# Performance work log

Measured on AMD Instinct MI355X. Metric: run time of the kernel, lower is better.

## Reference

```python
import jax, jax.numpy as jnp
import numpy as np

B, T, N, F = 8, 24, 207, 16
H = 64            # hidden_dim
DH = 16           # dims_hyper[-1] / node-embedding out
DA = 4 * F        # temporal attention dim_out
DS = 64           # ss_gal gcn out dim (last_ss_gal_dim)
GDEP = 2
ALPHA, BETA, GAMMA = 0.05, 0.95, 0.95
TA = 2.0


def _lin(x, w, b=None):
    y = x @ w
    return y if b is None else y + b


def gcn_hyper(x, A, W, b):
    # x: [B,N,C], A: [N,N] static. h <- a*x + g * einsum('nvc,vw->nwc', h, A)
    h = x
    outs = [h]
    for _ in range(GDEP):
        h = ALPHA * x + GAMMA * jnp.einsum('bvc,vw->bwc', h, A)
        outs.append(h)
    return _lin(jnp.concatenate(outs, axis=-1), W, b)


def gcn_gru(x, A_dyn, A_sta, W, b):
    # x: [B,N,C], A_dyn: [B,N,N], A_sta: [N,N]
    h = x
    outs = [h]
    for _ in range(GDEP):
        h = (ALPHA * x
             + BETA * jnp.einsum('bvw,bvc->bwc', A_dyn, h)     # bmm(A^T, h)
             + GAMMA * jnp.einsum('bvc,vw->bwc', h, A_sta))
        outs.append(h)
    return _lin(jnp.concatenate(outs, axis=-1), W, b)


def gcn_ssgal(x, A, W, b):
    # x: [B*,N,C], A: [B*,N,N]
    h = x
    outs = [h]
    for _ in range(GDEP):
        h = ALPHA * x + GAMMA * jnp.einsum('bvw,bvc->bwc', A, h)
        outs.append(h)
    return _lin(jnp.concatenate(outs, axis=-1), W, b)


def setup_inputs() -> dict:
    key = jax.random.key(0)
    ks = jax.random.split(key, 32)
    i = iter(range(32))
    w = lambda *s: (0.02 * jax.random.normal(ks[next(i)], s, dtype=jnp.float32))
    inp = {
        'input_sequence': jax.random.normal(ks[next(i)], (B, T, N, F), dtype=jnp.float32),
        'static_adj': jax.random.uniform(ks[next(i)], (N, N), dtype=jnp.float32),
        # hyper graph generators: mlp in = (GDEP+1)*H -> DH
        'src_gen_w': w((GDEP + 1) * H, DH), 'src_gen_b': w(DH),
        'tgt_gen_w': w((GDEP + 1) * H, DH), 'tgt_gen_b': w(DH),
        # node embeddings: F -> DH
        'src_emb_w': w(F, DH), 'src_emb_b': w(DH),
        'tgt_emb_w': w(F, DH), 'tgt_emb_b': w(DH),
        # GRU gate GCNs: mlp in = (GDEP+1)*(F+H) -> H
        'gru_z_w': w((GDEP + 1) * (F + H), H), 'gru_z_b': w(H),
        'gru_r_w': w((GDEP + 1) * (F + H), H), 'gru_r_b': w(H),
        'gru_c_w': w((GDEP + 1) * (F + H), H), 'gru_c_b': w(H),
        # temporal attention: F -> DA, score DA -> 1
        'attn_q_w': w(F, DA),
        'attn_k_w': w(F, DA), 'attn_k_b': w(DA),
        'attn_s_w': w(DA, 1),
        # ss_gal spatial gcn: (GDEP+1)*F -> DS
        'sgcn_w': w((GDEP + 1) * F, DS), 'sgcn_b': w(DS),
        # predictors
        'short_w': w(DS, F), 'short_b': w(F),
        'long_w': w(H, F), 'long_b': w(F),
        'fus_w': w(DS + H, F), 'fus_b': w(F),
    }
    return inp


def _forward(input_sequence, static_adj,
             src_gen_w, src_gen_b, tgt_gen_w, tgt_gen_b,
             src_emb_w, src_emb_b, tgt_emb_w, tgt_emb_b,
             gru_z_w, gru_z_b, gru_r_w, gru_r_b, gru_c_w, gru_c_b,
             attn_q_w, attn_k_w, attn_k_b, attn_s_w,
             sgcn_w, sgcn_b,
             short_w, short_b, long_w, long_b, fus_w, fus_b):
    batch, steps, nodes = input_sequence.shape[0], input_sequence.shape[1], input_sequence.shape[2]
    eye = jnp.eye(nodes, dtype=input_sequence.dtype)

    def cell(x_t, h):
        # x_t: [B,N,F], h: [B,N,H]
        src_ctx = gcn_hyper(h, static_adj, src_gen_w, src_gen_b)   # [B,N,DH]
        tgt_ctx = gcn_hyper(h, static_adj, tgt_gen_w, tgt_gen_b)
        s = jnp.tanh(TA * _lin(x_t, src_emb_w, src_emb_b) * src_ctx)
        t = jnp.tanh(TA * _lin(x_t, tgt_emb_w, tgt_emb_b) * tgt_ctx)
        asym = jnp.einsum('bnc,bmc->bnm', s, t) - jnp.einsum('bnc,bmc->bnm', t, s)
        adj = jax.nn.relu(jnp.tanh(TA * asym)) + eye
        adj = adj / (adj.sum(axis=-1, keepdims=True) + 1e-8)
        gi = jnp.concatenate([x_t, h], axis=-1)
        z = jax.nn.sigmoid(gcn_gru(gi, adj, static_adj, gru_z_w, gru_z_b))
        r = jax.nn.sigmoid(gcn_gru(gi, adj, static_adj, gru_r_w, gru_r_b))
        ri = jnp.concatenate([x_t, r * h], axis=-1)
        c = jnp.tanh(gcn_gru(ri, adj, static_adj, gru_c_w, gru_c_b))
        return z * h + (1.0 - z) * c

    h = jnp.zeros((batch, nodes, H), dtype=input_sequence.dtype)
    for t_step in range(0, max(1, steps - 4), 4):
        h = cell(input_sequence[:, t_step], h)

    # ss_gal branch on the last 4 steps
    recent = input_sequence[:, -4:]            # [B,4,N,F]
    target = input_sequence[:, -1]             # [B,N,F]
    # temporal attention
    q = target @ attn_q_w                      # [B,N,DA]
    k = recent @ attn_k_w + attn_k_b           # [B,4,N,DA]
    scores = jnp.tanh(q[:, None, :, None, :] + k[:, :, None, :, :])  # [B,4,N,N,DA]
    scores = jnp.squeeze(scores @ attn_s_w, axis=-1)                  # [B,4,N,N]
    attn = jax.nn.softmax(scores, axis=-1)
    dyn_adj = static_adj[None] + attn.reshape(-1, nodes, nodes)       # [B*4,N,N]
    rh = recent.reshape(-1, nodes, recent.shape[-1])                  # [B*4,N,F]
    rh = gcn_ssgal(rh, dyn_adj, sgcn_w, sgcn_b)                       # [B*4,N,DS]
    rh = jax.nn.relu(rh.reshape(batch, -1, nodes, rh.shape[-1]))      # [B,4,N,DS]
    target = jnp.sum(rh, axis=1)                                       # [B,N,DS]

    short = _lin(target, short_w, short_b)      # [B,N,F]
    h = cell(short, h)                          # final GRU step on short-term prediction
    long = _lin(h, long_w, long_b)              # [B,N,F]
    fused = _lin(jnp.concatenate([target, h], axis=-1), fus_w, fus_b)  # [B,N,F]
    return jnp.stack([short, long, fused], axis=0)  # [3,B,N,F]


def reference(input_sequence, static_adj,
              src_gen_w, src_gen_b, tgt_gen_w, tgt_gen_b,
              src_emb_w, src_emb_b, tgt_emb_w, tgt_emb_b,
              gru_z_w, gru_z_b, gru_r_w, gru_r_b, gru_c_w, gru_c_b,
              attn_q_w, attn_k_w, attn_k_b, attn_s_w,
              sgcn_w, sgcn_b,
              short_w, short_b, long_w, long_b, fus_w, fus_b):
    return _forward(input_sequence, static_adj,
                    src_gen_w, src_gen_b, tgt_gen_w, tgt_gen_b,
                    src_emb_w, src_emb_b, tgt_emb_w, tgt_emb_b,
                    gru_z_w, gru_z_b, gru_r_w, gru_r_b, gru_c_w, gru_c_b,
                    attn_q_w, attn_k_w, attn_k_b, attn_s_w,
                    sgcn_w, sgcn_b,
                    short_w, short_b, long_w, long_b, fus_w, fus_b)
```

## Files before the change

kernel.cpp:

```cpp
#include <hip/hip_runtime.h>


constexpr int B = 8, T = 24, N = 207, F = 16, H = 64, DH = 16;
constexpr int PS = 208;
constexpr float ALPHA = 0.05f, BETA = 0.95f, GAMMA = 0.95f, TA = 2.0f;
constexpr int NF = N * F;
constexpr int BNF = B * N * F;

__device__ __forceinline__ float tanh_fast(float x) { float e = __expf(2.f * x); return 1.f - 2.f / (e + 1.f); }
__device__ __forceinline__ float sigm(float x) { return 1.f / (1.f + __expf(-x)); }
__device__ __forceinline__ float tanh_pnc(float x) {
    float x2 = x * x;
    float p = x * (27.f + x2);
    float q = 27.f + 9.f * x2;
    return p * __builtin_amdgcn_rcpf(q);
}

__global__ __launch_bounds__(256) void k_build_Ts(const float* __restrict__ adj, float* __restrict__ Ts) {
    int i = blockIdx.x * 256 + threadIdx.x;
    if (i >= N * N) return;
    int w = i / N, v = i % N;
    Ts[(size_t)w * PS + v] = adj[v * N + w];
}

__global__ __launch_bounds__(256) void k_mm_sq(const float* __restrict__ Ain, float* __restrict__ Aout) {
    const float* A = Ain;
    float* O = Aout;
    int w0 = blockIdx.x * 32, v0b = blockIdx.y * 32;
    int tid = threadIdx.x;
    __shared__ float sA[2][32][33], sB[2][32][33];
    float acc[4] = {0, 0, 0, 0};
    int i0 = tid >> 5, j = tid & 31;
    int r = tid >> 3, c4 = (tid & 7) * 4;
    float4 av, bv;
    auto loadT = [&](int u0) {
        av = make_float4(0, 0, 0, 0); bv = make_float4(0, 0, 0, 0);
        int w = w0 + r, u = u0 + r;
        if (w < N) av = *(const float4*)&A[(size_t)w * PS + u0 + c4];
        if (u < N) bv = *(const float4*)&A[(size_t)u * PS + v0b + c4];
    };
    loadT(0);
    int cur = 0;
    for (int t = 0; t < 7; t++) {
        __syncthreads();
        sA[cur][r][c4] = av.x; sA[cur][r][c4 + 1] = av.y; sA[cur][r][c4 + 2] = av.z; sA[cur][r][c4 + 3] = av.w;
        sB[cur][r][c4] = bv.x; sB[cur][r][c4 + 1] = bv.y; sB[cur][r][c4 + 2] = bv.z; sB[cur][r][c4 + 3] = bv.w;
        if (t < 6) loadT((t + 1) * 32);
        __syncthreads();
#pragma unroll 8
        for (int u_ = 0; u_ < 32; u_++) {
            float bvv = sB[cur][u_][j];
#pragma unroll
            for (int k = 0; k < 4; k++) acc[k] += sA[cur][i0 + k * 8][u_] * bvv;
        }
        cur ^= 1;
    }
#pragma unroll
    for (int k = 0; k < 4; k++) {
        int w = w0 + i0 + k * 8, v = v0b + j;
        if (w < N && v < N) O[(size_t)w * PS + v] = acc[k];
    }
}

__global__ __launch_bounds__(256) void k_cell_a(
    const float* __restrict__ h, const float* __restrict__ Ts, const float* __restrict__ A2,
    const float* __restrict__ xseq, int tsel, const float* __restrict__ xbuf,
    const float* __restrict__ Wsrc, const float* __restrict__ bsrc,
    const float* __restrict__ Wtgt, const float* __restrict__ btgt,
    const float* __restrict__ Wes, const float* __restrict__ bes,
    const float* __restrict__ Wet, const float* __restrict__ bet,
    float* __restrict__ s_out, float* __restrict__ t_out, float* __restrict__ catg) {
    int b = blockIdx.y, w0 = blockIdx.x * 16;
    int tid = threadIdx.x, ty = tid >> 4, tx = tid & 15;
    __shared__ float sTs[2][16][33], sA2[2][16][33];
    __shared__ float sH[2][32][64];
    __shared__ float cat[16][193];
    __shared__ float sW[192][16];
    __shared__ float sX[16][16], sWe[16][16];
    float au[4] = {0, 0, 0, 0}, aw[4] = {0, 0, 0, 0};
    const float* hb = h + b * N * H;
    const float* xp = (tsel >= 0) ? (xseq + ((size_t)(b * T + tsel)) * NF) : (xbuf + (size_t)b * NF);
    int pidx = tid & 127;
    int pr = pidx >> 3, pc4 = (pidx & 7) * 4;
    float4 t4;
    float4 h4[2];
    int hr[2], hc[2];
#pragma unroll
    for (int k = 0; k < 2; k++) { int l4 = tid + k * 256; hr[k] = l4 >> 4; hc[k] = (l4 & 15) * 4; }
    auto loadT = [&](int v0) {
        t4 = make_float4(0, 0, 0, 0);
        const float* src = (tid < 128) ? Ts : A2;
        int w = w0 + pr;
        if (w < N) t4 = *(const float4*)&src[(size_t)w * PS + v0 + pc4];
#pragma unroll
        for (int k = 0; k < 2; k++) {
            float4 hv = make_float4(0, 0, 0, 0);
            int v = v0 + hr[k];
            if (v < N) hv = *(const float4*)&hb[(size_t)v * H + hc[k]];
            h4[k] = hv;
        }
    };
    loadT(0);
    int cur = 0;
    for (int t = 0; t < 7; t++) {
        __syncthreads();
        {
            float (*dst)[33] = (tid < 128) ? sTs[cur] : sA2[cur];
            dst[pr][pc4] = t4.x; dst[pr][pc4 + 1] = t4.y; dst[pr][pc4 + 2] = t4.z; dst[pr][pc4 + 3] = t4.w;
        }
#pragma unroll
        for (int k = 0; k < 2; k++) *(float4*)&sH[cur][hr[k]][hc[k]] = h4[k];
        if (t < 6) loadT((t + 1) * 32);
        __syncthreads();
#pragma unroll 8
        for (int v = 0; v < 32; v++) {
            float pu = sTs[cur][ty][v], pw = sA2[cur][ty][v];
#pragma unroll
            for (int j = 0; j < 4; j++) {
                float x = sH[cur][v][tx * 4 + j];
                au[j] += pu * x; aw[j] += pw * x;
            }
        }
        cur ^= 1;
    }
    int w = w0 + ty;
    bool valid = w < N;
    __syncthreads();
    if (valid) {
#pragma unroll
        for (int j = 0; j < 4; j++) {
            int c = tx * 4 + j;
            float hv = hb[w * H + c];
            float u = au[j], w2 = aw[j];
            cat[ty][c] = hv;
            cat[ty][64 + c] = ALPHA * hv + GAMMA * u;
            cat[ty][128 + c] = ALPHA * hv + ALPHA * GAMMA * u + GAMMA * GAMMA * w2;
        }
    } else {
#pragma unroll
        for (int j = 0; j < 4; j++) {
            int c = tx * 4 + j;
            cat[ty][c] = 0; cat[ty][64 + c] = 0; cat[ty][128 + c] = 0;
        }
    }
    {
        float4 wv[3];
#pragma unroll
        for (int k = 0; k < 3; k++) {
            int l4 = tid + k * 256;
            wv[k] = *(const float4*)&Wsrc[l4 * 4];
        }
        float4 xv = make_float4(0, 0, 0, 0), ev = make_float4(0, 0, 0, 0);
        int sr = 0, sc = 0;
        if (tid < 64) {
            sr = tid >> 2; sc = (tid & 3) * 4;
            int n = w0 + sr;
            if (n < N) xv = *(const float4*)&xp[(size_t)n * F + sc];
            ev = *(const float4*)&Wes[tid * 4];
        }
#pragma unroll
        for (int k = 0; k < 3; k++) {
            int l4 = tid + k * 256;
            int r = l4 >> 2, c4 = (l4 & 3) * 4;
            *(float4*)&sW[r][c4] = wv[k];
        }
        if (tid < 64) {
            *(float4*)&sX[sr][sc] = xv;
            *(float4*)&sWe[sr][sc] = ev;
        }
    }
    __syncthreads();
    if (valid) {
#pragma unroll
        for (int j = 0; j < 5; j++) {
            int c = tx * 5 + j;
            float v = (c < 16) ? sX[ty][c] : hb[w * H + (c - 16)];
            catg[((size_t)(b * N + w)) * 240 + c] = v;
        }
    }
    {
        float ctx = bsrc[tx];
#pragma unroll 8
        for (int c = 0; c < 192; c++) ctx += cat[ty][c] * sW[c][tx];
        float xe = bes[tx];
#pragma unroll
        for (int f = 0; f < 16; f++) xe += sX[ty][f] * sWe[f][tx];
        if (valid) s_out[(b * N + w) * DH + tx] = tanh_fast(TA * xe * ctx);
    }
    __syncthreads();
    {
        float4 wv[3];
#pragma unroll
        for (int k = 0; k < 3; k++) {
            int l4 = tid + k * 256;
            wv[k] = *(const float4*)&Wtgt[l4 * 4];
        }
        float4 ev = make_float4(0, 0, 0, 0);
        if (tid < 64) ev = *(const float4*)&Wet[tid * 4];
#pragma unroll
        for (int k = 0; k < 3; k++) {
            int l4 = tid + k * 256;
            int r = l4 >> 2, c4 = (l4 & 3) * 4;
            *(float4*)&sW[r][c4] = wv[k];
        }
        if (tid < 64) *(float4*)&sWe[tid >> 2][(tid & 3) * 4] = ev;
    }
    __syncthreads();
    {
        float ctx = btgt[tx];
#pragma unroll 8
        for (int c = 0; c < 192; c++) ctx += cat[ty][c] * sW[c][tx];
        float xe = bet[tx];
#pragma unroll
        for (int f = 0; f < 16; f++) xe += sX[ty][f] * sWe[f][tx];
        if (valid) t_out[(b * N + w) * DH + tx] = tanh_fast(TA * xe * ctx);
    }
}

__global__ __launch_bounds__(256) void k_cell_bP(const float* __restrict__ s_in, const float* __restrict__ t_in,
                                                 const float* __restrict__ adj, float* __restrict__ P) {
    int b = blockIdx.y, v0 = blockIdx.x * 16;
    int tid = threadIdx.x, ty = tid >> 4, tx = tid & 15;
    __shared__ float sS[N][17], sT[N][17];
    for (int l4 = tid; l4 < 828; l4 += 256) {
        float4 sv = *(const float4*)&s_in[(size_t)b * N * 16 + l4 * 4];
        float4 tv = *(const float4*)&t_in[(size_t)b * N * 16 + l4 * 4];
        int r = l4 >> 2, c = (l4 & 3) * 4;
        sS[r][c] = sv.x; sS[r][c + 1] = sv.y; sS[r][c + 2] = sv.z; sS[r][c + 3] = sv.w;
        sT[r][c] = tv.x; sT[r][c + 1] = tv.y; sT[r][c + 2] = tv.z; sT[r][c + 3] = tv.w;
    }
    __syncthreads();
    int v = v0 + ty;
    bool valid = v < N;
    int vc = valid ? v : (N - 1);
    float sv[16], tv[16];
#pragma unroll
    for (int k = 0; k < 16; k++) { sv[k] = sS[vc][k]; tv[k] = sT[vc][k]; }
    float val[13];
    float rsum = 0.f;
#pragma unroll
    for (int idx = 0; idx < 13; idx++) {
        int w = tx + 16 * idx;
        float r = 0.f;
        if (w < N) {
            float a = 0.f;
#pragma unroll
            for (int k = 0; k < 16; k++) a += sv[k] * sT[w][k] - tv[k] * sS[w][k];
            r = tanh_fast(TA * a);
            r = r > 0.f ? r : 0.f;
            if (w == v) r += 1.f;
        }
        val[idx] = r;
        rsum += r;
    }
    float tot = rsum;
    for (int d = 8; d > 0; d >>= 1) tot += __shfl_down(tot, d, 16);
    tot = __shfl(tot, 0, 16);
    float rinv = BETA / (tot + 1e-8f);
    if (valid) {
        float* Pb = P + (size_t)b * PS * PS;
#pragma unroll
        for (int idx = 0; idx < 13; idx++) {
            int w = tx + 16 * idx;
            if (w < N) Pb[(size_t)w * PS + v] = val[idx] * rinv + GAMMA * adj[v * N + w];
        }
    }
}

__global__ __launch_bounds__(256) void k_combineT(const float* __restrict__ Ain, const float* __restrict__ rs,
                                                  const float* __restrict__ Ts, float* __restrict__ Pout,
                                                  float cA, float cT) {
    int bt = blockIdx.z;
    int w0 = blockIdx.x * 32, v0 = blockIdx.y * 32;
    int tid = threadIdx.x;
    __shared__ float tile[32][33];
    __shared__ float rsv[32];
    int r = tid >> 3, c4 = (tid & 7) * 4;
    float4 a4 = make_float4(0, 0, 0, 0);
    int v = v0 + r;
    if (v < N) a4 = *(const float4*)&Ain[(size_t)bt * PS * PS + (size_t)v * PS + w0 + c4];
    tile[r][c4] = a4.x; tile[r][c4 + 1] = a4.y; tile[r][c4 + 2] = a4.z; tile[r][c4 + 3] = a4.w;
    if (tid < 32) {
        int vv = v0 + tid;
        rsv[tid] = (vv < N) ? (cA / rs[bt * N + vv]) : 0.f;
    }
    __syncthreads();
    for (int l = tid; l < 1024; l += 256) {
        int i = l >> 5, j = l & 31;
        int w = w0 + i, vv = v0 + j;
        if (w < N && vv < N)
            Pout[(size_t)bt * PS * PS + (size_t)w * PS + vv] = tile[j][i] * rsv[j] + cT * Ts[(size_t)w * PS + vv];
    }
}

__global__ __launch_bounds__(256) void k_prop1(const float* __restrict__ P, float* __restrict__ cat) {
    int b = blockIdx.y, w0 = blockIdx.x * 16, c0 = blockIdx.z * 16;
    int tid = threadIdx.x, ty = tid >> 4, tx = tid & 15;
    const float* Pb = P + (size_t)b * PS * PS;
    __shared__ float sP[2][16][33], sX[2][32][17];
    float a1 = 0.f;
    int pr = tid >> 4, pc = (tid & 15) * 2;
    int xr = tid >> 3, xc = (tid & 7) * 2;
    float2 pv, xv;
    auto loadT = [&](int v0) {
        pv = make_float2(0, 0); xv = make_float2(0, 0);
        int w = w0 + pr;
        if (w < N) pv = *(const float2*)&Pb[(size_t)w * PS + v0 + pc];
        int vv = v0 + xr;
        if (vv < N) xv = *(const float2*)&cat[((size_t)(b * N + vv)) * 240 + c0 + xc];
    };
    loadT(0);
    int cur = 0;
    for (int t = 0; t < 7; t++) {
        __syncthreads();
        sP[cur][pr][pc] = pv.x; sP[cur][pr][pc + 1] = pv.y;
        sX[cur][xr][xc] = xv.x; sX[cur][xr][xc + 1] = xv.y;
        if (t < 6) loadT((t + 1) * 32);
        __syncthreads();
#pragma unroll 8
        for (int v_ = 0; v_ < 32; v_++) a1 += sP[cur][ty][v_] * sX[cur][v_][tx];
        cur ^= 1;
    }
    int w = w0 + ty, c = c0 + tx;
    if (w < N) {
        size_t base = ((size_t)(b * N + w)) * 240;
        cat[base + 80 + c] = ALPHA * cat[base + c] + a1;
    }
}

__global__ __launch_bounds__(256) void k_gate(
    const float* __restrict__ cat, const float* __restrict__ P,
    const float* __restrict__ Wa, const float* __restrict__ ba,
    const float* __restrict__ Wb, const float* __restrict__ bb,
    int baseMode,
    const float* __restrict__ xseq, int tsel, const float* __restrict__ xbuf,
    float* __restrict__ zbuf, float* __restrict__ ricat,
    float* __restrict__ h,
    const float* __restrict__ target,
    const float* __restrict__ Wlong, const float* __restrict__ blong,
    const float* __restrict__ Wfus, const float* __restrict__ bfus,
    float* __restrict__ out) {
    int mode = baseMode + blockIdx.z;
    const float* W = (mode == 1) ? Wb : Wa;
    const float* bias = (mode == 1) ? bb : ba;
    int b = blockIdx.y, w0 = blockIdx.x * 16;
    int tid = threadIdx.x, ty = tid >> 4, tx = tid & 15;
    const float* Pb = P + (size_t)b * PS * PS;
    __shared__ float sC[16][241];
    __shared__ float sP[16][33];
    __shared__ float sX[32][81];
    __shared__ float sW[48][65];
    __shared__ float hrow[16][65], trow[16][65];
    for (int l4 = tid; l4 < 640; l4 += 256) {
        int r = l4 / 40, c4 = (l4 % 40) * 4;
        int w = w0 + r;
        float4 v4 = make_float4(0, 0, 0, 0);
        if (w < N) v4 = *(const float4*)&cat[((size_t)(b * N + w)) * 240 + c4];
        sC[r][c4] = v4.x; sC[r][c4 + 1] = v4.y; sC[r][c4 + 2] = v4.z; sC[r][c4 + 3] = v4.w;
    }
    float acc[5] = {0, 0, 0, 0, 0};
    int prr = tid >> 4, prc = (tid & 15) * 2;
    int xrow = tid & 31, xc0 = (tid >> 5) * 10;
    float2 pv;
    float2 xv[5];
    auto loadT = [&](int v0) {
        pv = make_float2(0, 0);
        int w = w0 + prr;
        if (w < N) pv = *(const float2*)&Pb[(size_t)w * PS + v0 + prc];
        int v = v0 + xrow;
#pragma unroll
        for (int k = 0; k < 5; k++) xv[k] = make_float2(0, 0);
        if (v < N) {
            const float* src = &cat[((size_t)(b * N + v)) * 240 + 80 + xc0];
#pragma unroll
            for (int k = 0; k < 5; k++) xv[k] = *(const float2*)&src[k * 2];
        }
    };
    loadT(0);
    for (int t = 0; t < 7; t++) {
        __syncthreads();
        sP[prr][prc] = pv.x; sP[prr][prc + 1] = pv.y;
#pragma unroll
        for (int k = 0; k < 5; k++) { sX[xrow][xc0 + 2 * k] = xv[k].x; sX[xrow][xc0 + 2 * k + 1] = xv[k].y; }
        if (t < 6) loadT((t + 1) * 32);
        __syncthreads();
#pragma unroll 8
        for (int v = 0; v < 32; v++) {
            float p = sP[ty][v];
#pragma unroll
            for (int j = 0; j < 5; j++) acc[j] += p * sX[v][tx * 5 + j];
        }
    }
#pragma unroll
    for (int j = 0; j < 5; j++) {
        int c = tx * 5 + j;
        sC[ty][160 + c] = ALPHA * sC[ty][c] + acc[j];
    }
    float4 wv[3];
#pragma unroll
    for (int k = 0; k < 3; k++) wv[k] = *(const float4*)&W[(tid + k * 256) * 4];
    float ga[4];
#pragma unroll
    for (int j = 0; j < 4; j++) ga[j] = bias[tx * 4 + j];
    for (int ch = 0; ch < 5; ch++) {
        __syncthreads();
#pragma unroll
        for (int k = 0; k < 3; k++) {
            int l4 = tid + k * 256;
            int r = l4 >> 4, cc = (l4 & 15) * 4;
            sW[r][cc] = wv[k].x; sW[r][cc + 1] = wv[k].y; sW[r][cc + 2] = wv[k].z; sW[r][cc + 3] = wv[k].w;
        }
        if (ch < 4) {
#pragma unroll
            for (int k = 0; k < 3; k++) wv[k] = *(const float4*)&W[(size_t)(ch + 1) * 48 * 64 + (tid + k * 256) * 4];
        }
        __syncthreads();
        int c0 = ch * 48;
#pragma unroll 8
        for (int cc = 0; cc < 48; cc++) {
            float cv = sC[ty][c0 + cc];
#pragma unroll
            for (int j = 0; j < 4; j++) ga[j] += cv * sW[cc][tx * 4 + j];
        }
    }
    int w = w0 + ty;
    bool valid = w < N;
    if (mode == 0) {
        if (valid) {
#pragma unroll
            for (int j = 0; j < 4; j++) zbuf[((size_t)(b * N + w)) * 64 + tx * 4 + j] = sigm(ga[j]);
        }
    } else if (mode == 1) {
        if (valid) {
#pragma unroll
            for (int j = 0; j < 4; j++) {
                int o = tx * 4 + j;
                ricat[((size_t)(b * N + w)) * 240 + 16 + o] = sigm(ga[j]) * h[((size_t)(b * N + w)) * 64 + o];
            }
            if (tx < 4) {
                const float* xp = (tsel >= 0) ? (xseq + ((size_t)(b * T + tsel)) * NF) : (xbuf + (size_t)b * NF);
#pragma unroll
                for (int j = 0; j < 4; j++) {
                    int c = tx * 4 + j;
                    ricat[((size_t)(b * N + w)) * 240 + c] = xp[w * F + c];
                }
            }
        }
    } else {
#pragma unroll
        for (int j = 0; j < 4; j++) {
            int o = tx * 4 + j;
            float cval = tanh_fast(ga[j]);
            float zv = 0.f, hv = 0.f;
            if (valid) { zv = zbuf[((size_t)(b * N + w)) * 64 + o]; hv = h[((size_t)(b * N + w)) * 64 + o]; }
            float hn = zv * hv + (1.f - zv) * cval;
            if (valid) h[((size_t)(b * N + w)) * 64 + o] = hn;
            hrow[ty][o] = valid ? hn : 0.f;
        }
        if (mode == 3) {
            for (int l = tid; l < 1024; l += 256) {
                int i = l >> 6, o = l & 63;
                int ww = w0 + i;
                trow[i][o] = (ww < N) ? target[((size_t)(b * N + ww)) * 64 + o] : 0.f;
            }
            __syncthreads();
            float lg = blong[tx];
            float fs = bfus[tx];
            for (int o = 0; o < 64; o++) {
                lg += hrow[ty][o] * Wlong[o * 16 + tx];
                fs += trow[ty][o] * Wfus[o * 16 + tx] + hrow[ty][o] * Wfus[(64 + o) * 16 + tx];
            }
            if (valid) {
                out[((size_t)1 * B * N + b * N + w) * 16 + tx] = lg;
                out[((size_t)2 * B * N + b * N + w) * 16 + tx] = fs;
            }
        }
    }
}

__global__ __launch_bounds__(256) void k_attn2(const float* __restrict__ inp,
                                               const float* __restrict__ Wq, const float* __restrict__ Wk,
                                               const float* __restrict__ kb, const float* __restrict__ sw_,
                                               float* __restrict__ attnU, float* __restrict__ rsum) {
    int bt = blockIdx.z, b = bt >> 2, tau = bt & 3;
    int n0 = blockIdx.x * 32, m0 = blockIdx.y * 32;
    int tid = threadIdx.x, ti = tid >> 4, tj = tid & 15;
    __shared__ float sQ[32][65], sK[32][65];
    __shared__ float sWq[16][64], sWk[16][64];
    __shared__ float sXq[32][17], sXk[32][17];
    __shared__ float ssw[64], skb[64];
    const float* xq = inp + ((size_t)(b * T + (T - 1))) * NF;
    const float* xk = inp + ((size_t)(b * T + 20 + tau)) * NF;
    {
        float4 wq4 = *(const float4*)&Wq[tid * 4];
        float4 wk4 = *(const float4*)&Wk[tid * 4];
        *(float4*)&sWq[tid >> 4][(tid & 15) * 4] = wq4;
        *(float4*)&sWk[tid >> 4][(tid & 15) * 4] = wk4;
        if (tid < 64) { ssw[tid] = sw_[tid]; skb[tid] = kb[tid]; }
        int idx = tid & 127;
        int r = idx >> 2, c4 = (idx & 3) * 4;
        if (tid < 128) {
            float4 a = make_float4(0, 0, 0, 0);
            int n = n0 + r;
            if (n < N) a = *(const float4*)&xq[(size_t)n * F + c4];
            sXq[r][c4] = a.x; sXq[r][c4 + 1] = a.y; sXq[r][c4 + 2] = a.z; sXq[r][c4 + 3] = a.w;
        } else {
            float4 c = make_float4(0, 0, 0, 0);
            int m = m0 + r;
            if (m < N) c = *(const float4*)&xk[(size_t)m * F + c4];
            sXk[r][c4] = c.x; sXk[r][c4 + 1] = c.y; sXk[r][c4 + 2] = c.z; sXk[r][c4 + 3] = c.w;
        }
    }
    __syncthreads();
    {
        int r = tid >> 3, o0 = (tid & 7) * 8;
        float xr[16], xkr[16];
#pragma unroll
        for (int f = 0; f < 16; f++) { xr[f] = sXq[r][f]; xkr[f] = sXk[r][f]; }
#pragma unroll
        for (int j = 0; j < 8; j++) {
            int o = o0 + j;
            float aq = 0.f, ak = skb[o];
#pragma unroll
            for (int f = 0; f < 16; f++) { aq += xr[f] * sWq[f][o]; ak += xkr[f] * sWk[f][o]; }
            sQ[r][o] = aq; sK[r][o] = ak;
        }
    }
    __syncthreads();
    float s00 = 0.f, s01 = 0.f, s10 = 0.f, s11 = 0.f;
#pragma unroll 2
    for (int d = 0; d < 64; d++) {
        float w = ssw[d];
        float q1 = sQ[ti][d], q2 = sQ[ti + 16][d];
        float k1 = sK[tj][d], k2 = sK[tj + 16][d];
        s00 += tanh_pnc(q1 + k1) * w;
        s01 += tanh_pnc(q1 + k2) * w;
        s10 += tanh_pnc(q2 + k1) * w;
        s11 += tanh_pnc(q2 + k2) * w;
    }
    int n1 = n0 + ti, n2 = n0 + ti + 16, m1 = m0 + tj, m2 = m0 + tj + 16;
    bool vn1 = n1 < N, vn2 = n2 < N, vm1 = m1 < N, vm2 = m2 < N;
    float e00 = (vn1 && vm1) ? __expf(s00) : 0.f;
    float e01 = (vn1 && vm2) ? __expf(s01) : 0.f;
    float e10 = (vn2 && vm1) ? __expf(s10) : 0.f;
    float e11 = (vn2 && vm2) ? __expf(s11) : 0.f;
    float part1 = e00 + e01, part2 = e10 + e11;
    for (int d = 8; d > 0; d >>= 1) {
        part1 += __shfl_down(part1, d, 16);
        part2 += __shfl_down(part2, d, 16);
    }
    if (tj == 0) {
        if (vn1) atomicAdd(&rsum[bt * N + n1], part1);
        if (vn2) atomicAdd(&rsum[bt * N + n2], part2);
    }
    size_t base = (size_t)bt * PS * PS;
    if (vn1 && vm1) attnU[base + (size_t)n1 * PS + m1] = e00;
    if (vn1 && vm2) attnU[base + (size_t)n1 * PS + m2] = e01;
    if (vn2 && vm1) attnU[base + (size_t)n2 * PS + m1] = e10;
    if (vn2 && vm2) attnU[base + (size_t)n2 * PS + m2] = e11;
}

__global__ __launch_bounds__(256) void k_prop_xr(const float* __restrict__ Pd, const float* __restrict__ inp,
                                                 float* __restrict__ x1) {
    int bt = blockIdx.y, w0 = blockIdx.x * 16;
    int b = bt >> 2, tau = bt & 3;
    const float* xb = inp + ((size_t)(b * T + 20 + tau)) * NF;
    const float* Pb = Pd + (size_t)bt * PS * PS;
    int tid = threadIdx.x, ty = tid >> 4, tx = tid & 15;
    __shared__ float sP[2][16][33];
    __shared__ float sX[2][32][17];
    float acc = 0.f;
    int prr = tid >> 3, pcc = (tid & 7) * 4;
    int xrr = (tid - 128) >> 2, xcc = ((tid - 128) & 3) * 4;
    float4 pv, xv;
    auto loadT = [&](int v0) {
        pv = make_float4(0, 0, 0, 0); xv = make_float4(0, 0, 0, 0);
        if (tid < 128) {
            int w = w0 + prr;
            if (w < N) pv = *(const float4*)&Pb[(size_t)w * PS + v0 + pcc];
        } else {
            int v = v0 + xrr;
            if (v < N) xv = *(const float4*)&xb[(size_t)v * F + xcc];
        }
    };
    loadT(0);
    int cur = 0;
    for (int t = 0; t < 7; t++) {
        __syncthreads();
        if (tid < 128) {
            sP[cur][prr][pcc] = pv.x; sP[cur][prr][pcc + 1] = pv.y; sP[cur][prr][pcc + 2] = pv.z; sP[cur][prr][pcc + 3] = pv.w;
        } else {
            sX[cur][xrr][xcc] = xv.x; sX[cur][xrr][xcc + 1] = xv.y; sX[cur][xrr][xcc + 2] = xv.z; sX[cur][xrr][xcc + 3] = xv.w;
        }
        if (t < 6) loadT((t + 1) * 32);
        __syncthreads();
#pragma unroll 8
        for (int v = 0; v < 32; v++) acc += sP[cur][ty][v] * sX[cur][v][tx];
        cur ^= 1;
    }
    int w = w0 + ty;
    if (w < N) x1[((size_t)(bt * N + w)) * 16 + tx] = ALPHA * xb[w * F + tx] + acc;
}

__global__ __launch_bounds__(256) void k_sgc2(const float* __restrict__ Pd, const float* __restrict__ x1,
                                              const float* __restrict__ inp,
                                              const float* __restrict__ Ws, const float* __restrict__ bs,
                                              float* __restrict__ target) {
    int bt = blockIdx.y, b = bt >> 2, tau = bt & 3, w0 = blockIdx.x * 16;
    const float* xb = inp + ((size_t)(b * T + 20 + tau)) * NF;
    const float* Pb = Pd + (size_t)bt * PS * PS;
    int tid = threadIdx.x, ty = tid >> 4, tx = tid & 15;
    __shared__ float sP[2][16][33], sX[2][32][17], cat[16][48], sW[48][64];
    float acc = 0.f;
    int prr = tid >> 3, pcc = (tid & 7) * 4;
    int xrr = (tid - 128) >> 2, xcc = ((tid - 128) & 3) * 4;
    float4 pv, xv;
    auto loadT = [&](int v0) {
        pv = make_float4(0, 0, 0, 0); xv = make_float4(0, 0, 0, 0);
        if (tid < 128) {
            int w = w0 + prr;
            if (w < N) pv = *(const float4*)&Pb[(size_t)w * PS + v0 + pcc];
        } else {
            int v = v0 + xrr;
            if (v < N) xv = *(const float4*)&x1[((size_t)(bt * N + v)) * 16 + xcc];
        }
    };
    loadT(0);
    int cur = 0;
    for (int t = 0; t < 7; t++) {
        __syncthreads();
        if (tid < 128) {
            sP[cur][prr][pcc] = pv.x; sP[cur][prr][pcc + 1] = pv.y; sP[cur][prr][pcc + 2] = pv.z; sP[cur][prr][pcc + 3] = pv.w;
        } else {
            sX[cur][xrr][xcc] = xv.x; sX[cur][xrr][xcc + 1] = xv.y; sX[cur][xrr][xcc + 2] = xv.z; sX[cur][xrr][xcc + 3] = xv.w;
        }
        if (t < 6) loadT((t + 1) * 32);
        __syncthreads();
#pragma unroll 8
        for (int v = 0; v < 32; v++) acc += sP[cur][ty][v] * sX[cur][v][tx];
        cur ^= 1;
    }
    int w = w0 + ty;
    bool valid = w < N;
    __syncthreads();
    for (int l = tid; l < 512; l += 256) {
        int i = l >> 5, c = l & 31;
        int ww = w0 + i;
        float vv = 0;
        if (ww < N) {
            if (c < 16) vv = xb[ww * F + c];
            else vv = x1[((size_t)bt * N + ww) * 16 + (c - 16)];
        }
        cat[i][c] = vv;
    }
    {
        float x0 = valid ? xb[w * F + tx] : 0.f;
        cat[ty][32 + tx] = ALPHA * x0 + acc;
    }
    {
        float4 wv[3];
#pragma unroll
        for (int k = 0; k < 3; k++) wv[k] = *(const float4*)&Ws[(tid + k * 256) * 4];
#pragma unroll
        for (int k = 0; k < 3; k++) {
            int l4 = tid + k * 256;
            *(float4*)&sW[l4 >> 4][(l4 & 15) * 4] = wv[k];
        }
    }
    __syncthreads();
    float a[4];
#pragma unroll
    for (int j = 0; j < 4; j++) a[j] = bs[tx * 4 + j];
#pragma unroll 8
    for (int cc = 0; cc < 48; cc++) {
        float cv = cat[ty][cc];
#pragma unroll
        for (int j = 0; j < 4; j++) a[j] += cv * sW[cc][tx * 4 + j];
    }
    if (valid) {
#pragma unroll
        for (int j = 0; j < 4; j++) {
            float r = a[j] > 0.f ? a[j] : 0.f;
            atomicAdd(&target[(b * N + w) * 64 + tx * 4 + j], r);
        }
    }
}

__global__ __launch_bounds__(256) void k_short(const float* __restrict__ target,
                                               const float* __restrict__ Wsh, const float* __restrict__ bsh,
                                               float* __restrict__ out, float* __restrict__ xshort) {
    int b = blockIdx.y, n0 = blockIdx.x * 16;
    int tid = threadIdx.x, ty = tid >> 4, tx = tid & 15;
    __shared__ float trow[16][65], sW[64][16];
    {
        int r = tid >> 4, c4 = (tid & 15) * 4;
        int n = n0 + r;
        float4 tv = make_float4(0, 0, 0, 0);
        if (n < N) tv = *(const float4*)&target[((size_t)(b * N + n)) * 64 + c4];
        trow[r][c4] = tv.x; trow[r][c4 + 1] = tv.y; trow[r][c4 + 2] = tv.z; trow[r][c4 + 3] = tv.w;
        float4 wv = *(const float4*)&Wsh[tid * 4];
        *(float4*)&sW[tid >> 2][(tid & 3) * 4] = wv;
    }
    __syncthreads();
    float a = bsh[tx];
#pragma unroll 8
    for (int o = 0; o < 64; o++) a += trow[ty][o] * sW[o][tx];
    int n = n0 + ty;
    if (n < N) {
        out[((size_t)0 * B * N + b * N + n) * 16 + tx] = a;
        xshort[(b * N + n) * 16 + tx] = a;
    }
}

extern "C" void kernel_launch(void* const* d_in, const int* in_sizes, int n_in,
                              void* d_out, int out_size, void* d_ws, size_t ws_size,
                              hipStream_t stream) {
    const float* inp = (const float*)d_in[0];
    const float* adj = (const float*)d_in[1];
    const float* src_gen_w = (const float*)d_in[2];
    const float* src_gen_b = (const float*)d_in[3];
    const float* tgt_gen_w = (const float*)d_in[4];
    const float* tgt_gen_b = (const float*)d_in[5];
    const float* src_emb_w = (const float*)d_in[6];
    const float* src_emb_b = (const float*)d_in[7];
    const float* tgt_emb_w = (const float*)d_in[8];
    const float* tgt_emb_b = (const float*)d_in[9];
    const float* gru_z_w = (const float*)d_in[10];
    const float* gru_z_b = (const float*)d_in[11];
    const float* gru_r_w = (const float*)d_in[12];
    const float* gru_r_b = (const float*)d_in[13];
    const float* gru_c_w = (const float*)d_in[14];
    const float* gru_c_b = (const float*)d_in[15];
    const float* attn_q_w = (const float*)d_in[16];
    const float* attn_k_w = (const float*)d_in[17];
    const float* attn_k_b = (const float*)d_in[18];
    const float* attn_s_w = (const float*)d_in[19];
    const float* sgcn_w = (const float*)d_in[20];
    const float* sgcn_b = (const float*)d_in[21];
    const float* short_w = (const float*)d_in[22];
    const float* short_b = (const float*)d_in[23];
    const float* long_w = (const float*)d_in[24];
    const float* long_b = (const float*)d_in[25];
    const float* fus_w = (const float*)d_in[26];
    const float* fus_b = (const float*)d_in[27];
    float* out = (float*)d_out;

    float* ws = (float*)d_ws;
    size_t off = 0;
    auto A = [&](size_t n) { n = (n + 3) & ~(size_t)3; float* p = ws + off; off += n; return p; };
    float* Ts = A((size_t)PS * PS);
    float* A2 = A((size_t)PS * PS);
    float* h = A((size_t)B * N * H);
    float* sbuf = A((size_t)B * N * DH);
    float* tbuf = A((size_t)B * N * DH);
    float* P = A((size_t)B * PS * PS);
    float* catg = A((size_t)B * N * 240);
    float* catc = A((size_t)B * N * 240);
    float* zb = A((size_t)B * N * 64);
    float* attnU = A((size_t)32 * PS * PS);
    float* Pd = A((size_t)32 * PS * PS);
    float* x1 = A((size_t)32 * NF);
    float* target = A((size_t)B * N * 64);
    float* rsum = A((size_t)32 * N);
    float* xshort = A(BNF);
    (void)ws_size; (void)in_sizes; (void)n_in; (void)out_size;

    hipMemsetAsync(h, 0, sizeof(float) * B * N * H, stream);
    hipMemsetAsync(target, 0, sizeof(float) * (B * N * 64), stream);
    hipMemsetAsync(rsum, 0, sizeof(float) * (32 * N), stream);
    k_build_Ts<<<(N * N + 255) / 256, 256, 0, stream>>>(adj, Ts);
    k_mm_sq<<<dim3(7, 7), 256, 0, stream>>>(Ts, A2);

    auto run_cell = [&](int tsel, const float* xbuf, int finalFlag) {
        k_cell_a<<<dim3(13, B), 256, 0, stream>>>(h, Ts, A2, inp, tsel, xbuf,
                                                  src_gen_w, src_gen_b, tgt_gen_w, tgt_gen_b,
                                                  src_emb_w, src_emb_b, tgt_emb_w, tgt_emb_b, sbuf, tbuf, catg);
        k_cell_bP<<<dim3(13, B), 256, 0, stream>>>(sbuf, tbuf, adj, P);
        k_prop1<<<dim3(13, B, 5), 256, 0, stream>>>(P, catg);
        k_gate<<<dim3(13, B, 2), 256, 0, stream>>>(catg, P, gru_z_w, gru_z_b, gru_r_w, gru_r_b, 0,
                                                   inp, tsel, xbuf, zb, catc, h,
                                                   nullptr, nullptr, nullptr, nullptr, nullptr, nullptr);
        k_prop1<<<dim3(13, B, 5), 256, 0, stream>>>(P, catc);
        k_gate<<<dim3(13, B, 1), 256, 0, stream>>>(catc, P, gru_c_w, gru_c_b, nullptr, nullptr, 2 + finalFlag,
                                                   nullptr, 0, nullptr, zb, nullptr, h,
                                                   target, long_w, long_b, fus_w, fus_b, out);
    };

    for (int t = 0; t < 20; t += 4) run_cell(t, nullptr, 0);

    k_attn2<<<dim3(7, 7, 32), 256, 0, stream>>>(inp, attn_q_w, attn_k_w, attn_k_b, attn_s_w, attnU, rsum);
    k_combineT<<<dim3(7, 7, 32), 256, 0, stream>>>(attnU, rsum, Ts, Pd, GAMMA, GAMMA);
    k_prop_xr<<<dim3(13, 32), 256, 0, stream>>>(Pd, inp, x1);
    k_sgc2<<<dim3(13, 32), 256, 0, stream>>>(Pd, x1, inp, sgcn_w, sgcn_b, target);
    k_short<<<dim3(13, B), 256, 0, stream>>>(target, short_w, short_b, out, xshort);

    run_cell(-1, xshort, 1);
}
```

Baseline: 661.6 us.

## Fuse GRU cell kernels into persistent megakernel with per-batch atomic barriers

Replaces the six-kernel-per-step GRU cell sequence (cell_a, cell_bP, prop, gate, prop, gate) with one persistent kernel per run of cells. Blocks of each batch (13x2) coordinate through atomic-counter grid barriers, and z-gate values stay in registers instead of a global buffer. The goal is to remove roughly 30 kernel launches and their gaps, plus global round-trips. It relies on all 208 blocks being co-resident to avoid deadlock, and it adds barrier spin overhead. The memsets are also merged into one.

```diff
diff --git a/kernel.cpp b/kernel.cpp
--- a/kernel.cpp
+++ b/kernel.cpp
@@ -14,6 +14,18 @@
     float p = x * (27.f + x2);
     float q = 27.f + 9.f * x2;
     return p * __builtin_amdgcn_rcpf(q);
+}
+
+__device__ __forceinline__ void bbar(unsigned* slot) {
+    __syncthreads();
+    if (threadIdx.x == 0) {
+        __threadfence();
+        __hip_atomic_fetch_add(slot, 1u, __ATOMIC_ACQ_REL, __HIP_MEMORY_SCOPE_AGENT);
+        while (__hip_atomic_load(slot, __ATOMIC_ACQUIRE, __HIP_MEMORY_SCOPE_AGENT) < 26u)
+            __builtin_amdgcn_s_sleep(2);
+        __threadfence();
+    }
+    __syncthreads();
 }
 
 __global__ __launch_bounds__(256) void k_build_Ts(const float* __restrict__ adj, float* __restrict__ Ts) {
@@ -62,419 +74,359 @@
     }
 }
 
-__global__ __launch_bounds__(256) void k_cell_a(
-    const float* __restrict__ h, const float* __restrict__ Ts, const float* __restrict__ A2,
-    const float* __restrict__ xseq, int tsel, const float* __restrict__ xbuf,
+__global__ __launch_bounds__(256) void k_mega(
+    int ncells, int t0, const float* __restrict__ xbuf, int finalFlag,
+    unsigned* __restrict__ bars, int barBase,
+    const float* __restrict__ inp, const float* __restrict__ adj,
+    const float* __restrict__ Ts, const float* __restrict__ A2,
     const float* __restrict__ Wsrc, const float* __restrict__ bsrc,
     const float* __restrict__ Wtgt, const float* __restrict__ btgt,
     const float* __restrict__ Wes, const float* __restrict__ bes,
     const float* __restrict__ Wet, const float* __restrict__ bet,
-    float* __restrict__ s_out, float* __restrict__ t_out, float* __restrict__ catg) {
-    int b = blockIdx.y, w0 = blockIdx.x * 16;
-    int tid = threadIdx.x, ty = tid >> 4, tx = tid & 15;
-    __shared__ float sTs[2][16][33], sA2[2][16][33];
-    __shared__ float sH[2][32][64];
-    __shared__ float cat[16][193];
-    __shared__ float sW[192][16];
-    __shared__ float sX[16][16], sWe[16][16];
-    float au[4] = {0, 0, 0, 0}, aw[4] = {0, 0, 0, 0};
-    const float* hb = h + b * N * H;
-    const float* xp = (tsel >= 0) ? (xseq + ((size_t)(b * T + tsel)) * NF) : (xbuf + (size_t)b * NF);
-    int pidx = tid & 127;
-    int pr = pidx >> 3, pc4 = (pidx & 7) * 4;
-    float4 t4;
-    float4 h4[2];
-    int hr[2], hc[2];
-#pragma unroll
-    for (int k = 0; k < 2; k++) { int l4 = tid + k * 256; hr[k] = l4 >> 4; hc[k] = (l4 & 15) * 4; }
-    auto loadT = [&](int v0) {
-        t4 = make_float4(0, 0, 0, 0);
-        const float* src = (tid < 128) ? Ts : A2;
-        int w = w0 + pr;
-        if (w < N) t4 = *(const float4*)&src[(size_t)w * PS + v0 + pc4];
-#pragma unroll
-        for (int k = 0; k < 2; k++) {
-            float4 hv = make_float4(0, 0, 0, 0);
-            int v = v0 + hr[k];
-            if (v < N) hv = *(const float4*)&hb[(size_t)v * H + hc[k]];
-            h4[k] = hv;
-        }
-    };
-    loadT(0);
-    int cur = 0;
-    for (int t = 0; t < 7; t++) {
-        __syncthreads();
-        {
-            float (*dst)[33] = (tid < 128) ? sTs[cur] : sA2[cur];
-            dst[pr][pc4] = t4.x; dst[pr][pc4 + 1] = t4.y; dst[pr][pc4 + 2] = t4.z; dst[pr][pc4 + 3] = t4.w;
-        }
-#pragma unroll
-        for (int k = 0; k < 2; k++) *(float4*)&sH[cur][hr[k]][hc[k]] = h4[k];
-        if (t < 6) loadT((t + 1) * 32);
-        __syncthreads();
-#pragma unroll 8
-        for (int v = 0; v < 32; v++) {
-            float pu = sTs[cur][ty][v], pw = sA2[cur][ty][v];
-#pragma unroll
-            for (int j = 0; j < 4; j++) {
-                float x = sH[cur][v][tx * 4 + j];
-                au[j] += pu * x; aw[j] += pw * x;
-            }
-        }
-        cur ^= 1;
-    }
-    int w = w0 + ty;
-    bool valid = w < N;
-    __syncthreads();
-    if (valid) {
-#pragma unroll
-        for (int j = 0; j < 4; j++) {
-            int c = tx * 4 + j;
-            float hv = hb[w * H + c];
-            float u = au[j], w2 = aw[j];
-            cat[ty][c] = hv;
-            cat[ty][64 + c] = ALPHA * hv + GAMMA * u;
-            cat[ty][128 + c] = ALPHA * hv + ALPHA * GAMMA * u + GAMMA * GAMMA * w2;
-        }
-    } else {
-#pragma unroll
-        for (int j = 0; j < 4; j++) {
-            int c = tx * 4 + j;
-            cat[ty][c] = 0; cat[ty][64 + c] = 0; cat[ty][128 + c] = 0;
-        }
-    }
-    {
-        float4 wv[3];
-#pragma unroll
-        for (int k = 0; k < 3; k++) {
-            int l4 = tid + k * 256;
-            wv[k] = *(const float4*)&Wsrc[l4 * 4];
-        }
-        float4 xv = make_float4(0, 0, 0, 0), ev = make_float4(0, 0, 0, 0);
-        int sr = 0, sc = 0;
-        if (tid < 64) {
-            sr = tid >> 2; sc = (tid & 3) * 4;
-            int n = w0 + sr;
-            if (n < N) xv = *(const float4*)&xp[(size_t)n * F + sc];
-            ev = *(const float4*)&Wes[tid * 4];
-        }
-#pragma unroll
-        for (int k = 0; k < 3; k++) {
-            int l4 = tid + k * 256;
-            int r = l4 >> 2, c4 = (l4 & 3) * 4;
-            *(float4*)&sW[r][c4] = wv[k];
-        }
-        if (tid < 64) {
-            *(float4*)&sX[sr][sc] = xv;
-            *(float4*)&sWe[sr][sc] = ev;
-        }
-    }
-    __syncthreads();
-    if (valid) {
-#pragma unroll
-        for (int j = 0; j < 5; j++) {
-            int c = tx * 5 + j;
-            float v = (c < 16) ? sX[ty][c] : hb[w * H + (c - 16)];
-            catg[((size_t)(b * N + w)) * 240 + c] = v;
-        }
-    }
-    {
-        float ctx = bsrc[tx];
-#pragma unroll 8
-        for (int c = 0; c < 192; c++) ctx += cat[ty][c] * sW[c][tx];
-        float xe = bes[tx];
-#pragma unroll
-        for (int f = 0; f < 16; f++) xe += sX[ty][f] * sWe[f][tx];
-        if (valid) s_out[(b * N + w) * DH + tx] = tanh_fast(TA * xe * ctx);
-    }
-    __syncthreads();
-    {
-        float4 wv[3];
-#pragma unroll
-        for (int k = 0; k < 3; k++) {
-            int l4 = tid + k * 256;
-            wv[k] = *(const float4*)&Wtgt[l4 * 4];
-        }
-        float4 ev = make_float4(0, 0, 0, 0);
-        if (tid < 64) ev = *(const float4*)&Wet[tid * 4];
-#pragma unroll
-        for (int k = 0; k < 3; k++) {
-            int l4 = tid + k * 256;
-            int r = l4 >> 2, c4 = (l4 & 3) * 4;
-            *(float4*)&sW[r][c4] = wv[k];
-        }
-        if (tid < 64) *(float4*)&sWe[tid >> 2][(tid & 3) * 4] = ev;
-    }
-    __syncthreads();
-    {
-        float ctx = btgt[tx];
-#pragma unroll 8
-        for (int c = 0; c < 192; c++) ctx += cat[ty][c] * sW[c][tx];
-        float xe = bet[tx];
-#pragma unroll
-        for (int f = 0; f < 16; f++) xe += sX[ty][f] * sWe[f][tx];
-        if (valid) t_out[(b * N + w) * DH + tx] = tanh_fast(TA * xe * ctx);
-    }
-}
-
-__global__ __launch_bounds__(256) void k_cell_bP(const float* __restrict__ s_in, const float* __restrict__ t_in,
-                                                 const float* __restrict__ adj, float* __restrict__ P) {
-    int b = blockIdx.y, v0 = blockIdx.x * 16;
-    int tid = threadIdx.x, ty = tid >> 4, tx = tid & 15;
-    __shared__ float sS[N][17], sT[N][17];
-    for (int l4 = tid; l4 < 828; l4 += 256) {
-        float4 sv = *(const float4*)&s_in[(size_t)b * N * 16 + l4 * 4];
-        float4 tv = *(const float4*)&t_in[(size_t)b * N * 16 + l4 * 4];
-        int r = l4 >> 2, c = (l4 & 3) * 4;
-        sS[r][c] = sv.x; sS[r][c + 1] = sv.y; sS[r][c + 2] = sv.z; sS[r][c + 3] = sv.w;
-        sT[r][c] = tv.x; sT[r][c + 1] = tv.y; sT[r][c + 2] = tv.z; sT[r][c + 3] = tv.w;
-    }
-    __syncthreads();
-    int v = v0 + ty;
-    bool valid = v < N;
-    int vc = valid ? v : (N - 1);
-    float sv[16], tv[16];
-#pragma unroll
-    for (int k = 0; k < 16; k++) { sv[k] = sS[vc][k]; tv[k] = sT[vc][k]; }
-    float val[13];
-    float rsum = 0.f;
-#pragma unroll
-    for (int idx = 0; idx < 13; idx++) {
-        int w = tx + 16 * idx;
-        float r = 0.f;
-        if (w < N) {
-            float a = 0.f;
-#pragma unroll
-            for (int k = 0; k < 16; k++) a += sv[k] * sT[w][k] - tv[k] * sS[w][k];
-            r = tanh_fast(TA * a);
-            r = r > 0.f ? r : 0.f;
-            if (w == v) r += 1.f;
-        }
-        val[idx] = r;
-        rsum += r;
-    }
-    float tot = rsum;
-    for (int d = 8; d > 0; d >>= 1) tot += __shfl_down(tot, d, 16);
-    tot = __shfl(tot, 0, 16);
-    float rinv = BETA / (tot + 1e-8f);
-    if (valid) {
-        float* Pb = P + (size_t)b * PS * PS;
-#pragma unroll
-        for (int idx = 0; idx < 13; idx++) {
-            int w = tx + 16 * idx;
-            if (w < N) Pb[(size_t)w * PS + v] = val[idx] * rinv + GAMMA * adj[v * N + w];
-        }
-    }
-}
-
-__global__ __launch_bounds__(256) void k_combineT(const float* __restrict__ Ain, const float* __restrict__ rs,
-                                                  const float* __restrict__ Ts, float* __restrict__ Pout,
-                                                  float cA, float cT) {
-    int bt = blockIdx.z;
-    int w0 = blockIdx.x * 32, v0 = blockIdx.y * 32;
-    int tid = threadIdx.x;
-    __shared__ float tile[32][33];
-    __shared__ float rsv[32];
-    int r = tid >> 3, c4 = (tid & 7) * 4;
-    float4 a4 = make_float4(0, 0, 0, 0);
-    int v = v0 + r;
-    if (v < N) a4 = *(const float4*)&Ain[(size_t)bt * PS * PS + (size_t)v * PS + w0 + c4];
-    tile[r][c4] = a4.x; tile[r][c4 + 1] = a4.y; tile[r][c4 + 2] = a4.z; tile[r][c4 + 3] = a4.w;
-    if (tid < 32) {
-        int vv = v0 + tid;
-        rsv[tid] = (vv < N) ? (cA / rs[bt * N + vv]) : 0.f;
-    }
-    __syncthreads();
-    for (int l = tid; l < 1024; l += 256) {
-        int i = l >> 5, j = l & 31;
-        int w = w0 + i, vv = v0 + j;
-        if (w < N && vv < N)
-            Pout[(size_t)bt * PS * PS + (size_t)w * PS + vv] = tile[j][i] * rsv[j] + cT * Ts[(size_t)w * PS + vv];
-    }
-}
-
-__global__ __launch_bounds__(256) void k_prop1(const float* __restrict__ P, float* __restrict__ cat) {
-    int b = blockIdx.y, w0 = blockIdx.x * 16, c0 = blockIdx.z * 16;
-    int tid = threadIdx.x, ty = tid >> 4, tx = tid & 15;
-    const float* Pb = P + (size_t)b * PS * PS;
-    __shared__ float sP[2][16][33], sX[2][32][17];
-    float a1 = 0.f;
-    int pr = tid >> 4, pc = (tid & 15) * 2;
-    int xr = tid >> 3, xc = (tid & 7) * 2;
-    float2 pv, xv;
-    auto loadT = [&](int v0) {
-        pv = make_float2(0, 0); xv = make_float2(0, 0);
-        int w = w0 + pr;
-        if (w < N) pv = *(const float2*)&Pb[(size_t)w * PS + v0 + pc];
-        int vv = v0 + xr;
-        if (vv < N) xv = *(const float2*)&cat[((size_t)(b * N + vv)) * 240 + c0 + xc];
-    };
-    loadT(0);
-    int cur = 0;
-    for (int t = 0; t < 7; t++) {
-        __syncthreads();
-        sP[cur][pr][pc] = pv.x; sP[cur][pr][pc + 1] = pv.y;
-        sX[cur][xr][xc] = xv.x; sX[cur][xr][xc + 1] = xv.y;
-        if (t < 6) loadT((t + 1) * 32);
-        __syncthreads();
-#pragma unroll 8
-        for (int v_ = 0; v_ < 32; v_++) a1 += sP[cur][ty][v_] * sX[cur][v_][tx];
-        cur ^= 1;
-    }
-    int w = w0 + ty, c = c0 + tx;
-    if (w < N) {
-        size_t base = ((size_t)(b * N + w)) * 240;
-        cat[base + 80 + c] = ALPHA * cat[base + c] + a1;
-    }
-}
-
-__global__ __launch_bounds__(256) void k_gate(
-    const float* __restrict__ cat, const float* __restrict__ P,
-    const float* __restrict__ Wa, const float* __restrict__ ba,
-    const float* __restrict__ Wb, const float* __restrict__ bb,
-    int baseMode,
-    const float* __restrict__ xseq, int tsel, const float* __restrict__ xbuf,
-    float* __restrict__ zbuf, float* __restrict__ ricat,
-    float* __restrict__ h,
-    const float* __restrict__ target,
+    const float* __restrict__ Wz, const float* __restrict__ bz,
+    const float* __restrict__ Wr, const float* __restrict__ br,
+    const float* __restrict__ Wc, const float* __restrict__ bc,
     const float* __restrict__ Wlong, const float* __restrict__ blong,
     const float* __restrict__ Wfus, const float* __restrict__ bfus,
-    float* __restrict__ out) {
-    int mode = baseMode + blockIdx.z;
-    const float* W = (mode == 1) ? Wb : Wa;
-    const float* bias = (mode == 1) ? bb : ba;
-    int b = blockIdx.y, w0 = blockIdx.x * 16;
-    int tid = threadIdx.x, ty = tid >> 4, tx = tid & 15;
-    const float* Pb = P + (size_t)b * PS * PS;
-    __shared__ float sC[16][241];
-    __shared__ float sP[16][33];
-    __shared__ float sX[32][81];
-    __shared__ float sW[48][65];
-    __shared__ float hrow[16][65], trow[16][65];
-    for (int l4 = tid; l4 < 640; l4 += 256) {
-        int r = l4 / 40, c4 = (l4 % 40) * 4;
-        int w = w0 + r;
-        float4 v4 = make_float4(0, 0, 0, 0);
-        if (w < N) v4 = *(const float4*)&cat[((size_t)(b * N + w)) * 240 + c4];
-        sC[r][c4] = v4.x; sC[r][c4 + 1] = v4.y; sC[r][c4 + 2] = v4.z; sC[r][c4 + 3] = v4.w;
-    }
-    float acc[5] = {0, 0, 0, 0, 0};
-    int prr = tid >> 4, prc = (tid & 15) * 2;
-    int xrow = tid & 31, xc0 = (tid >> 5) * 10;
-    float2 pv;
-    float2 xv[5];
-    auto loadT = [&](int v0) {
-        pv = make_float2(0, 0);
-        int w = w0 + prr;
-        if (w < N) pv = *(const float2*)&Pb[(size_t)w * PS + v0 + prc];
-        int v = v0 + xrow;
-#pragma unroll
-        for (int k = 0; k < 5; k++) xv[k] = make_float2(0, 0);
-        if (v < N) {
-            const float* src = &cat[((size_t)(b * N + v)) * 240 + 80 + xc0];
-#pragma unroll
-            for (int k = 0; k < 5; k++) xv[k] = *(const float2*)&src[k * 2];
+    float* __restrict__ h, float* __restrict__ sbuf, float* __restrict__ tbuf,
+    float* __restrict__ P, float* __restrict__ catg, float* __restrict__ catc,
+    const float* __restrict__ target, float* __restrict__ out)
+{
+    __shared__ __align__(16) float smem[13312];
+    const int wb = blockIdx.x, b = blockIdx.y, lane = blockIdx.z;
+    const int tid = threadIdx.x, ty = tid >> 4, tx = tid & 15;
+    const int w0 = wb * 16;
+    unsigned* bb = bars + b * 96 + barBase;
+    int bi = 0;
+    float* hb = h + (size_t)b * N * H;
+    float* Pb = P + (size_t)b * PS * PS;
+    float zreg[4] = {0.f, 0.f, 0.f, 0.f};
+
+    auto prop = [&](float* cat, int srcOff, int dstOff) {
+        float* sP = smem;
+        float* sX = smem + 16 * 208;
+        for (int l4 = tid; l4 < 832; l4 += 256) {
+            int r = l4 / 52, c4 = (l4 % 52) * 4;
+            float4 v = make_float4(0.f, 0.f, 0.f, 0.f);
+            int w = w0 + r;
+            if (w < N) v = *(const float4*)&Pb[(size_t)w * PS + c4];
+            *(float4*)&sP[r * 208 + c4] = v;
+        }
+        int cbase = srcOff + lane * 40;
+        for (int l4 = tid; l4 < 2080; l4 += 256) {
+            int r = l4 / 10, q = (l4 % 10) * 4;
+            float4 v = make_float4(0.f, 0.f, 0.f, 0.f);
+            if (r < N) v = *(const float4*)&cat[((size_t)(b * N + r)) * 240 + cbase + q];
+            *(float4*)&sX[r * 48 + q] = v;
+        }
+        __syncthreads();
+        if (tid < 16) sP[tid * 208 + 207] = 0.f;
+        __syncthreads();
+        float acc0 = 0.f, acc1 = 0.f, acc2 = 0.f;
+        for (int v = 0; v < 208; v += 4) {
+#pragma unroll
+            for (int u = 0; u < 4; u++) {
+                float p = sP[ty * 208 + v + u];
+                const float* xr = &sX[(v + u) * 48];
+                acc0 += p * xr[tx];
+                acc1 += p * xr[16 + tx];
+                acc2 += p * xr[32 + tx];
+            }
+        }
+        int w = w0 + ty;
+        if (w < N) {
+            size_t row = ((size_t)(b * N + w)) * 240;
+            int cl = lane * 40;
+            cat[row + dstOff + cl + tx] = ALPHA * cat[row + cl + tx] + acc0;
+            cat[row + dstOff + cl + 16 + tx] = ALPHA * cat[row + cl + 16 + tx] + acc1;
+            if (tx < 8) cat[row + dstOff + cl + 32 + tx] = ALPHA * cat[row + cl + 32 + tx] + acc2;
         }
     };
-    loadT(0);
-    for (int t = 0; t < 7; t++) {
-        __syncthreads();
-        sP[prr][prc] = pv.x; sP[prr][prc + 1] = pv.y;
-#pragma unroll
-        for (int k = 0; k < 5; k++) { sX[xrow][xc0 + 2 * k] = xv[k].x; sX[xrow][xc0 + 2 * k + 1] = xv[k].y; }
-        if (t < 6) loadT((t + 1) * 32);
-        __syncthreads();
-#pragma unroll 8
-        for (int v = 0; v < 32; v++) {
-            float p = sP[ty][v];
-#pragma unroll
-            for (int j = 0; j < 5; j++) acc[j] += p * sX[v][tx * 5 + j];
-        }
-    }
-#pragma unroll
-    for (int j = 0; j < 5; j++) {
-        int c = tx * 5 + j;
-        sC[ty][160 + c] = ALPHA * sC[ty][c] + acc[j];
-    }
-    float4 wv[3];
-#pragma unroll
-    for (int k = 0; k < 3; k++) wv[k] = *(const float4*)&W[(tid + k * 256) * 4];
-    float ga[4];
-#pragma unroll
-    for (int j = 0; j < 4; j++) ga[j] = bias[tx * 4 + j];
-    for (int ch = 0; ch < 5; ch++) {
-        __syncthreads();
-#pragma unroll
-        for (int k = 0; k < 3; k++) {
-            int l4 = tid + k * 256;
-            int r = l4 >> 4, cc = (l4 & 15) * 4;
-            sW[r][cc] = wv[k].x; sW[r][cc + 1] = wv[k].y; sW[r][cc + 2] = wv[k].z; sW[r][cc + 3] = wv[k].w;
-        }
-        if (ch < 4) {
-#pragma unroll
-            for (int k = 0; k < 3; k++) wv[k] = *(const float4*)&W[(size_t)(ch + 1) * 48 * 64 + (tid + k * 256) * 4];
-        }
-        __syncthreads();
-        int c0 = ch * 48;
-#pragma unroll 8
-        for (int cc = 0; cc < 48; cc++) {
-            float cv = sC[ty][c0 + cc];
-#pragma unroll
-            for (int j = 0; j < 4; j++) ga[j] += cv * sW[cc][tx * 4 + j];
-        }
-    }
-    int w = w0 + ty;
-    bool valid = w < N;
-    if (mode == 0) {
-        if (valid) {
-#pragma unroll
-            for (int j = 0; j < 4; j++) zbuf[((size_t)(b * N + w)) * 64 + tx * 4 + j] = sigm(ga[j]);
-        }
-    } else if (mode == 1) {
-        if (valid) {
+
+    auto gate = [&](const float* cat, const float* W, const float* bias, float* ga) {
+        float* sC = smem;
+        float* sW = smem + 3856;
+        for (int l4 = tid; l4 < 960; l4 += 256) {
+            int r = l4 / 60, c4 = (l4 % 60) * 4;
+            float4 v = make_float4(0.f, 0.f, 0.f, 0.f);
+            int w = w0 + r;
+            if (w < N) v = *(const float4*)&cat[((size_t)(b * N + w)) * 240 + c4];
+            sC[r * 241 + c4] = v.x; sC[r * 241 + c4 + 1] = v.y; sC[r * 241 + c4 + 2] = v.z; sC[r * 241 + c4 + 3] = v.w;
+        }
+        float4 wv[3];
+#pragma unroll
+        for (int k = 0; k < 3; k++) wv[k] = *(const float4*)&W[(tid + k * 256) * 4];
+#pragma unroll
+        for (int j = 0; j < 4; j++) ga[j] = bias[tx * 4 + j];
+        for (int ch = 0; ch < 5; ch++) {
+            __syncthreads();
+#pragma unroll
+            for (int k = 0; k < 3; k++) {
+                int l4 = tid + k * 256;
+                int r = l4 >> 4, cc = (l4 & 15) * 4;
+                sW[r * 65 + cc] = wv[k].x; sW[r * 65 + cc + 1] = wv[k].y;
+                sW[r * 65 + cc + 2] = wv[k].z; sW[r * 65 + cc + 3] = wv[k].w;
+            }
+            if (ch < 4) {
+#pragma unroll
+                for (int k = 0; k < 3; k++) wv[k] = *(const float4*)&W[(size_t)(ch + 1) * 3072 + (tid + k * 256) * 4];
+            }
+            __syncthreads();
+            int c0 = ch * 48;
+#pragma unroll 8
+            for (int cc = 0; cc < 48; cc++) {
+                float cv = sC[ty * 241 + c0 + cc];
+#pragma unroll
+                for (int j = 0; j < 4; j++) ga[j] += cv * sW[cc * 65 + tx * 4 + j];
+            }
+        }
+    };
+
+    for (int cell = 0; cell < ncells; cell++) {
+        int tsel = (t0 >= 0) ? (t0 + 4 * cell) : -1;
+        const float* xp = (tsel >= 0) ? (inp + ((size_t)(b * T + tsel)) * NF) : (xbuf + (size_t)b * NF);
+
+        {
+            float au[4] = {0, 0, 0, 0}, aw[4] = {0, 0, 0, 0};
+            int pidx = tid & 127;
+            int pr = pidx >> 3, pc4 = (pidx & 7) * 4;
+            float4 t4;
+            float4 h4[2];
+            int hr[2], hc[2];
+#pragma unroll
+            for (int k = 0; k < 2; k++) { int l4 = tid + k * 256; hr[k] = l4 >> 4; hc[k] = (l4 & 15) * 4; }
+            auto loadT = [&](int v0) {
+                t4 = make_float4(0, 0, 0, 0);
+                const float* src = (tid < 128) ? Ts : A2;
+                int w = w0 + pr;
+                if (w < N) t4 = *(const float4*)&src[(size_t)w * PS + v0 + pc4];
+#pragma unroll
+                for (int k = 0; k < 2; k++) {
+                    float4 hv = make_float4(0, 0, 0, 0);
+                    int v = v0 + hr[k];
+                    if (v < N) hv = *(const float4*)&hb[(size_t)v * H + hc[k]];
+                    h4[k] = hv;
+                }
+            };
+            loadT(0);
+            int cur = 0;
+            for (int t = 0; t < 7; t++) {
+                __syncthreads();
+                {
+                    float* dst = (tid < 128) ? (smem + cur * 528) : (smem + 1056 + cur * 528);
+                    dst[pr * 33 + pc4] = t4.x; dst[pr * 33 + pc4 + 1] = t4.y;
+                    dst[pr * 33 + pc4 + 2] = t4.z; dst[pr * 33 + pc4 + 3] = t4.w;
+                }
+#pragma unroll
+                for (int k = 0; k < 2; k++) *(float4*)&smem[2112 + cur * 2048 + hr[k] * 64 + hc[k]] = h4[k];
+                if (t < 6) loadT((t + 1) * 32);
+                __syncthreads();
+#pragma unroll 8
+                for (int v = 0; v < 32; v++) {
+                    float pu = smem[cur * 528 + ty * 33 + v];
+                    float pw = smem[1056 + cur * 528 + ty * 33 + v];
+#pragma unroll
+                    for (int j = 0; j < 4; j++) {
+                        float x = smem[2112 + cur * 2048 + v * 64 + tx * 4 + j];
+                        au[j] += pu * x; aw[j] += pw * x;
+                    }
+                }
+                cur ^= 1;
+            }
+            int w = w0 + ty;
+            bool valid = w < N;
+            __syncthreads();
+            float* catL = smem + 6208;
+            if (valid) {
+#pragma unroll
+                for (int j = 0; j < 4; j++) {
+                    int c = tx * 4 + j;
+                    float hv = hb[(size_t)w * H + c];
+                    float u = au[j], w2 = aw[j];
+                    catL[ty * 193 + c] = hv;
+                    catL[ty * 193 + 64 + c] = ALPHA * hv + GAMMA * u;
+                    catL[ty * 193 + 128 + c] = ALPHA * hv + ALPHA * GAMMA * u + GAMMA * GAMMA * w2;
+                }
+            } else {
+#pragma unroll
+                for (int j = 0; j < 4; j++) {
+                    int c = tx * 4 + j;
+                    catL[ty * 193 + c] = 0; catL[ty * 193 + 64 + c] = 0; catL[ty * 193 + 128 + c] = 0;
+                }
+            }
+            const float* Wg = lane ? Wtgt : Wsrc;
+            const float* bg = lane ? btgt : bsrc;
+            const float* We = lane ? Wet : Wes;
+            const float* be = lane ? bet : bes;
+            {
+                float4 wv[3];
+#pragma unroll
+                for (int k = 0; k < 3; k++) wv[k] = *(const float4*)&Wg[(tid + k * 256) * 4];
+                float4 xv = make_float4(0, 0, 0, 0), ev = make_float4(0, 0, 0, 0);
+                int sr = 0, sc = 0;
+                if (tid < 64) {
+                    sr = tid >> 2; sc = (tid & 3) * 4;
+                    int n = w0 + sr;
+                    if (n < N) xv = *(const float4*)&xp[(size_t)n * F + sc];
+                    ev = *(const float4*)&We[tid * 4];
+                }
+#pragma unroll
+                for (int k = 0; k < 3; k++) {
+                    int l4 = tid + k * 256;
+                    int r = l4 >> 2, c4 = (l4 & 3) * 4;
+                    *(float4*)&smem[9296 + r * 16 + c4] = wv[k];
+                }
+                if (tid < 64) {
+                    *(float4*)&smem[12368 + sr * 16 + sc] = xv;
+                    *(float4*)&smem[12624 + sr * 16 + sc] = ev;
+                }
+            }
+            __syncthreads();
+            if (lane == 0 && valid) {
+#pragma unroll
+                for (int j = 0; j < 5; j++) {
+                    int c = tx * 5 + j;
+                    float v = (c < 16) ? smem[12368 + ty * 16 + c] : hb[(size_t)w * H + (c - 16)];
+                    catg[((size_t)(b * N + w)) * 240 + c] = v;
+                }
+            }
+            {
+                float ctx = bg[tx];
+#pragma unroll 8
+                for (int c = 0; c < 192; c++) ctx += catL[ty * 193 + c] * smem[9296 + c * 16 + tx];
+                float xe = be[tx];
+#pragma unroll
+                for (int f = 0; f < 16; f++) xe += smem[12368 + ty * 16 + f] * smem[12624 + f * 16 + tx];
+                if (valid) {
+                    float val = tanh_fast(TA * xe * ctx);
+                    if (lane == 0) sbuf[(size_t)(b * N + w) * DH + tx] = val;
+                    else           tbuf[(size_t)(b * N + w) * DH + tx] = val;
+                }
+            }
+        }
+        bbar(&bb[bi++]);
+
+        if (lane == 0) {
+            float* sS = smem;
+            float* sT = smem + 3519;
+            for (int l4 = tid; l4 < 828; l4 += 256) {
+                float4 sv = *(const float4*)&sbuf[(size_t)b * N * 16 + l4 * 4];
+                float4 tv = *(const float4*)&tbuf[(size_t)b * N * 16 + l4 * 4];
+                int r = l4 >> 2, c = (l4 & 3) * 4;
+                sS[r * 17 + c] = sv.x; sS[r * 17 + c + 1] = sv.y; sS[r * 17 + c + 2] = sv.z; sS[r * 17 + c + 3] = sv.w;
+                sT[r * 17 + c] = tv.x; sT[r * 17 + c + 1] = tv.y; sT[r * 17 + c + 2] = tv.z; sT[r * 17 + c + 3] = tv.w;
+            }
+            __syncthreads();
+            int v = w0 + ty;
+            bool valid = v < N;
+            int vc = valid ? v : (N - 1);
+            float sv[16], tv[16];
+#pragma unroll
+            for (int k = 0; k < 16; k++) { sv[k] = sS[vc * 17 + k]; tv[k] = sT[vc * 17 + k]; }
+            float val[13];
+            float rsum = 0.f;
+#pragma unroll
+            for (int idx = 0; idx < 13; idx++) {
+                int w = tx + 16 * idx;
+                float r = 0.f;
+                if (w < N) {
+                    float a = 0.f;
+#pragma unroll
+                    for (int k = 0; k < 16; k++) a += sv[k] * sT[w * 17 + k] - tv[k] * sS[w * 17 + k];
+                    r = tanh_fast(TA * a);
+                    r = r > 0.f ? r : 0.f;
+                    if (w == v) r += 1.f;
+                }
+                val[idx] = r;
+                rsum += r;
+            }
+            float tot = rsum;
+            for (int d = 8; d > 0; d >>= 1) tot += __shfl_down(tot, d, 16);
+            tot = __shfl(tot, 0, 16);
+            float rinv = BETA / (tot + 1e-8f);
+            if (valid) {
+#pragma unroll
+                for (int idx = 0; idx < 13; idx++) {
+                    int w = tx + 16 * idx;
+                    if (w < N) Pb[(size_t)w * PS + v] = val[idx] * rinv + GAMMA * adj[v * N + w];
+                }
+            }
+        }
+        bbar(&bb[bi++]);
+
+        prop(catg, 0, 80);
+        bbar(&bb[bi++]);
+        prop(catg, 80, 160);
+        bbar(&bb[bi++]);
+
+        {
+            float ga[4];
+            if (lane == 0) {
+                gate(catg, Wz, bz, ga);
+#pragma unroll
+                for (int j = 0; j < 4; j++) zreg[j] = sigm(ga[j]);
+            } else {
+                gate(catg, Wr, br, ga);
+                int w = w0 + ty;
+                if (w < N) {
+#pragma unroll
+                    for (int j = 0; j < 4; j++) {
+                        int o = tx * 4 + j;
+                        catc[((size_t)(b * N + w)) * 240 + 16 + o] = sigm(ga[j]) * hb[(size_t)w * H + o];
+                    }
+                    if (tx < 4) {
+#pragma unroll
+                        for (int j = 0; j < 4; j++) {
+                            int c = tx * 4 + j;
+                            catc[((size_t)(b * N + w)) * 240 + c] = xp[w * F + c];
+                        }
+                    }
+                }
+            }
+        }
+        bbar(&bb[bi++]);
+
+        prop(catc, 0, 80);
+        bbar(&bb[bi++]);
+        prop(catc, 80, 160);
+        bbar(&bb[bi++]);
+
+        if (lane == 0) {
+            float ga[4];
+            gate(catc, Wc, bc, ga);
+            float* hrow = smem + 6976;
+            float* trow = smem + 8016;
+            int w = w0 + ty;
+            bool valid = w < N;
 #pragma unroll
             for (int j = 0; j < 4; j++) {
                 int o = tx * 4 + j;
-                ricat[((size_t)(b * N + w)) * 240 + 16 + o] = sigm(ga[j]) * h[((size_t)(b * N + w)) * 64 + o];
-            }
-            if (tx < 4) {
-                const float* xp = (tsel >= 0) ? (xseq + ((size_t)(b * T + tsel)) * NF) : (xbuf + (size_t)b * NF);
-#pragma unroll
-                for (int j = 0; j < 4; j++) {
-                    int c = tx * 4 + j;
-                    ricat[((size_t)(b * N + w)) * 240 + c] = xp[w * F + c];
-                }
-            }
-        }
-    } else {
-#pragma unroll
-        for (int j = 0; j < 4; j++) {
-            int o = tx * 4 + j;
-            float cval = tanh_fast(ga[j]);
-            float zv = 0.f, hv = 0.f;
-            if (valid) { zv = zbuf[((size_t)(b * N + w)) * 64 + o]; hv = h[((size_t)(b * N + w)) * 64 + o]; }
-            float hn = zv * hv + (1.f - zv) * cval;
-            if (valid) h[((size_t)(b * N + w)) * 64 + o] = hn;
-            hrow[ty][o] = valid ? hn : 0.f;
-        }
-        if (mode == 3) {
-            for (int l = tid; l < 1024; l += 256) {
-                int i = l >> 6, o = l & 63;
-                int ww = w0 + i;
-                trow[i][o] = (ww < N) ? target[((size_t)(b * N + ww)) * 64 + o] : 0.f;
-            }
-            __syncthreads();
-            float lg = blong[tx];
-            float fs = bfus[tx];
-            for (int o = 0; o < 64; o++) {
-                lg += hrow[ty][o] * Wlong[o * 16 + tx];
-                fs += trow[ty][o] * Wfus[o * 16 + tx] + hrow[ty][o] * Wfus[(64 + o) * 16 + tx];
-            }
-            if (valid) {
-                out[((size_t)1 * B * N + b * N + w) * 16 + tx] = lg;
-                out[((size_t)2 * B * N + b * N + w) * 16 + tx] = fs;
-            }
-        }
+                float cval = tanh_fast(ga[j]);
+                float hv = valid ? hb[(size_t)w * H + o] : 0.f;
+                float hn = zreg[j] * hv + (1.f - zreg[j]) * cval;
+                if (valid) hb[(size_t)w * H + o] = hn;
+                hrow[ty * 65 + o] = valid ? hn : 0.f;
+            }
+            if (finalFlag && cell == ncells - 1) {
+                for (int l = tid; l < 1024; l += 256) {
+                    int i = l >> 6, o = l & 63;
+                    int ww = w0 + i;
+                    trow[i * 65 + o] = (ww < N) ? target[((size_t)(b * N + ww)) * 64 + o] : 0.f;
+                }
+                __syncthreads();
+                float lg = blong[tx], fs = bfus[tx];
+#pragma unroll 8
+                for (int o = 0; o < 64; o++) {
+                    lg += hrow[ty * 65 + o] * Wlong[o * 16 + tx];
+                    fs += trow[ty * 65 + o] * Wfus[o * 16 + tx] + hrow[ty * 65 + o] * Wfus[(64 + o) * 16 + tx];
+                }
+                if (valid) {
+                    out[((size_t)1 * B * N + b * N + w) * 16 + tx] = lg;
+                    out[((size_t)2 * B * N + b * N + w) * 16 + tx] = fs;
+                }
+            }
+        }
+        bbar(&bb[bi++]);
     }
 }
 
@@ -558,6 +510,32 @@
     if (vn1 && vm2) attnU[base + (size_t)n1 * PS + m2] = e01;
     if (vn2 && vm1) attnU[base + (size_t)n2 * PS + m1] = e10;
     if (vn2 && vm2) attnU[base + (size_t)n2 * PS + m2] = e11;
+}
+
+__global__ __launch_bounds__(256) void k_combineT(const float* __restrict__ Ain, const float* __restrict__ rs,
+                                                  const float* __restrict__ Ts, float* __restrict__ Pout,
+                                                  float cA, float cT) {
+    int bt = blockIdx.z;
+    int w0 = blockIdx.x * 32, v0 = blockIdx.y * 32;
+    int tid = threadIdx.x;
+    __shared__ float tile[32][33];
+    __shared__ float rsv[32];
+    int r = tid >> 3, c4 = (tid & 7) * 4;
+    float4 a4 = make_float4(0, 0, 0, 0);
+    int v = v0 + r;
+    if (v < N) a4 = *(const float4*)&Ain[(size_t)bt * PS * PS + (size_t)v * PS + w0 + c4];
+    tile[r][c4] = a4.x; tile[r][c4 + 1] = a4.y; tile[r][c4 + 2] = a4.z; tile[r][c4 + 3] = a4.w;
+    if (tid < 32) {
+        int vv = v0 + tid;
+        rsv[tid] = (vv < N) ? (cA / rs[bt * N + vv]) : 0.f;
+    }
+    __syncthreads();
+    for (int l = tid; l < 1024; l += 256) {
+        int i = l >> 5, j = l & 31;
+        int w = w0 + i, vv = v0 + j;
+        if (w < N && vv < N)
+            Pout[(size_t)bt * PS * PS + (size_t)w * PS + vv] = tile[j][i] * rsv[j] + cT * Ts[(size_t)w * PS + vv];
+    }
 }
 
 __global__ __launch_bounds__(256) void k_prop_xr(const float* __restrict__ Pd, const float* __restrict__ inp,
@@ -750,43 +728,35 @@
     auto A = [&](size_t n) { n = (n + 3) & ~(size_t)3; float* p = ws + off; off += n; return p; };
     float* Ts = A((size_t)PS * PS);
     float* A2 = A((size_t)PS * PS);
-    float* h = A((size_t)B * N * H);
     float* sbuf = A((size_t)B * N * DH);
     float* tbuf = A((size_t)B * N * DH);
     float* P = A((size_t)B * PS * PS);
     float* catg = A((size_t)B * N * 240);
     float* catc = A((size_t)B * N * 240);
-    float* zb = A((size_t)B * N * 64);
     float* attnU = A((size_t)32 * PS * PS);
     float* Pd = A((size_t)32 * PS * PS);
     float* x1 = A((size_t)32 * NF);
+    float* xshort = A(BNF);
+    size_t zero_begin = off;
+    float* h = A((size_t)B * N * H);
     float* target = A((size_t)B * N * 64);
     float* rsum = A((size_t)32 * N);
-    float* xshort = A(BNF);
+    float* barsf = A((size_t)8 * 96);
+    size_t zero_end = off;
+    unsigned* bars = (unsigned*)barsf;
     (void)ws_size; (void)in_sizes; (void)n_in; (void)out_size;
 
-    hipMemsetAsync(h, 0, sizeof(float) * B * N * H, stream);
-    hipMemsetAsync(target, 0, sizeof(float) * (B * N * 64), stream);
-    hipMemsetAsync(rsum, 0, sizeof(float) * (32 * N), stream);
+    hipMemsetAsync(h, 0, (zero_end - zero_begin) * sizeof(float), stream);
     k_build_Ts<<<(N * N + 255) / 256, 256, 0, stream>>>(adj, Ts);
     k_mm_sq<<<dim3(7, 7), 256, 0, stream>>>(Ts, A2);
 
-    auto run_cell = [&](int tsel, const float* xbuf, int finalFlag) {
-        k_cell_a<<<dim3(13, B), 256, 0, stream>>>(h, Ts, A2, inp, tsel, xbuf,
-                                                  src_gen_w, src_gen_b, tgt_gen_w, tgt_gen_b,
-                                                  src_emb_w, src_emb_b, tgt_emb_w, tgt_emb_b, sbuf, tbuf, catg);
-        k_cell_bP<<<dim3(13, B), 256, 0, stream>>>(sbuf, tbuf, adj, P);
-        k_prop1<<<dim3(13, B, 5), 256, 0, stream>>>(P, catg);
-        k_gate<<<dim3(13, B, 2), 256, 0, stream>>>(catg, P, gru_z_w, gru_z_b, gru_r_w, gru_r_b, 0,
-                                                   inp, tsel, xbuf, zb, catc, h,
-                                                   nullptr, nullptr, nullptr, nullptr, nullptr, nullptr);
-        k_prop1<<<dim3(13, B, 5), 256, 0, stream>>>(P, catc);
-        k_gate<<<dim3(13, B, 1), 256, 0, stream>>>(catc, P, gru_c_w, gru_c_b, nullptr, nullptr, 2 + finalFlag,
-                                                   nullptr, 0, nullptr, zb, nullptr, h,
-                                                   target, long_w, long_b, fus_w, fus_b, out);
-    };
-
-    for (int t = 0; t < 20; t += 4) run_cell(t, nullptr, 0);
+    k_mega<<<dim3(13, 8, 2), 256, 0, stream>>>(
+        5, 0, nullptr, 0, bars, 0,
+        inp, adj, Ts, A2,
+        src_gen_w, src_gen_b, tgt_gen_w, tgt_gen_b, src_emb_w, src_emb_b, tgt_emb_w, tgt_emb_b,
+        gru_z_w, gru_z_b, gru_r_w, gru_r_b, gru_c_w, gru_c_b,
+        long_w, long_b, fus_w, fus_b,
+        h, sbuf, tbuf, P, catg, catc, target, out);
 
     k_attn2<<<dim3(7, 7, 32), 256, 0, stream>>>(inp, attn_q_w, attn_k_w, attn_k_b, attn_s_w, attnU, rsum);
     k_combineT<<<dim3(7, 7, 32), 256, 0, stream>>>(attnU, rsum, Ts, Pd, GAMMA, GAMMA);
@@ -794,5 +764,11 @@
     k_sgc2<<<dim3(13, 32), 256, 0, stream>>>(Pd, x1, inp, sgcn_w, sgcn_b, target);
     k_short<<<dim3(13, B), 256, 0, stream>>>(target, short_w, short_b, out, xshort);
 
-    run_cell(-1, xshort, 1);
-}
+    k_mega<<<dim3(13, 8, 2), 256, 0, stream>>>(
+        1, -1, xshort, 1, bars, 48,
+        inp, adj, Ts, A2,
+        src_gen_w, src_gen_b, tgt_gen_w, tgt_gen_b, src_emb_w, src_emb_b, tgt_emb_w, tgt_emb_b,
+        gru_z_w, gru_z_b, gru_r_w, gru_r_b, gru_c_w, gru_c_b,
+        long_w, long_b, fus_w, fus_b,
+        h, sbuf, tbuf, P, catg, catc, target, out);
+}
```

Measured after the change: 1.804 ms. 2.73x slower.
